# Kernel tuning notes

Hardware: AMD Instinct MI355X
Metric: run time of the kernel (lower is better)

Reference implementation:

```python
import jax, jax.numpy as jnp
import numpy as np

K_BASE = 8
K_MAX = 20
NUM_GROUPS = 16  # min(32, 64 // 4)
EPS = 1e-5


def _knn_idx_adaptive(x, mask, k_base=K_BASE, k_max=K_MAX):
    # x: [B, N, D] float, mask: [B, N] bool. Returns idx: [B, N, k_max] int32.
    B, N, D = x.shape
    x2 = jnp.sum(x * x, axis=-1, keepdims=True)              # [B, N, 1]
    dist2 = x2 + x2.transpose(0, 2, 1) - 2.0 * jnp.einsum('bnd,bmd->bnm', x, x)
    dist2 = jnp.clip(dist2, 0.0)
    valid = mask[:, :, None] & mask[:, None, :]
    eye = jnp.eye(N, dtype=bool)[None]
    dist2 = jnp.where(valid & ~eye, dist2, jnp.inf)
    counts = mask.sum(axis=1)                                 # [B]
    k_per = jnp.clip(jnp.sqrt(counts.astype(jnp.float32) / 50.0) * k_base,
                     k_base, k_max).astype(jnp.int32)         # truncation == torch .long()
    k_global = jnp.minimum(k_max, jnp.maximum(1, counts.min() - 1))
    _, idx = jax.lax.top_k(-dist2, k_max)                     # [B, N, k_max]
    first_valid = jnp.argmax(mask, axis=1)                    # [B]
    cols = jnp.arange(k_max)[None, None, :]
    k_eff = jnp.minimum(k_per, k_global)[:, None, None]
    # cols < k_eff: true top-k neighbors; [k_eff, k_global): repeat first valid; >= k_global: pad 0
    idx = jnp.where(cols < k_eff, idx,
                    jnp.where(cols < k_global, first_valid[:, None, None], 0))
    return idx


def _group_norm(h, gamma, beta, num_groups=NUM_GROUPS, eps=EPS):
    # h: [..., C]
    shp = h.shape
    C = shp[-1]
    hg = h.reshape(shp[:-1] + (num_groups, C // num_groups))
    mu = hg.mean(axis=-1, keepdims=True)
    var = hg.var(axis=-1, keepdims=True)
    hg = (hg - mu) * jax.lax.rsqrt(var + eps)
    return hg.reshape(shp) * gamma + beta


def setup_inputs() -> dict:
    key = jax.random.key(0)
    kx, kl, k1, k2 = jax.random.split(key, 4)
    B, N, D, C = 16, 1024, 64, 64
    x = jax.random.normal(kx, (B, N, D), dtype=jnp.float32)
    lengths = jax.random.randint(kl, (B,), 256, N + 1)
    mask = jnp.arange(N)[None, :] < lengths[:, None]          # [B, N] bool
    W1 = jax.random.normal(k1, (2 * D, C), dtype=jnp.float32) / np.sqrt(2 * D)
    b1 = jnp.zeros((C,), dtype=jnp.float32)
    gamma = jnp.ones((C,), dtype=jnp.float32)
    beta = jnp.zeros((C,), dtype=jnp.float32)
    W2 = jax.random.normal(k2, (C, C), dtype=jnp.float32) / np.sqrt(C)
    b2 = jnp.zeros((C,), dtype=jnp.float32)
    return {"x": x, "mask": mask, "W1": W1, "b1": b1,
            "gamma": gamma, "beta": beta, "W2": W2, "b2": b2}


def reference(x, mask, W1, b1, gamma, beta, W2, b2):
    B, N, D = x.shape
    idx = _knn_idx_adaptive(x, mask)                          # [B, N, k]
    k = idx.shape[-1]
    x_nb = jnp.take_along_axis(x[:, :, None, :].repeat(1, axis=2),
                               idx[..., None], axis=1) if False else \
        x[jnp.arange(B)[:, None, None], idx]                  # [B, N, k, D]
    x_i = jnp.broadcast_to(x[:, :, None, :], (B, N, k, D))
    edge = jnp.concatenate([x_i, x_nb - x_i], axis=-1)        # [B, N, k, 2D]
    h = jax.nn.relu(_group_norm(edge @ W1 + b1, gamma, beta)) # [B, N, k, C]
    h = h @ W2 + b2
    out = h.max(axis=2)                                       # [B, N, C]
    return out * mask[..., None].astype(out.dtype)
```

## Files before the change

kernel.cpp:

```cpp
#include <hip/hip_runtime.h>
#include <stdint.h>

#define BB 16
#define NN 1024
#define DD 64
#define CC 64
#define KMAX 20
#define ROWS 8

typedef unsigned long long u64;
typedef float f32x2 __attribute__((ext_vector_type(2)));
typedef float f32x4v __attribute__((ext_vector_type(4)));
typedef short bf16x8 __attribute__((ext_vector_type(8)));

__device__ inline u64 umin64(u64 a, u64 b) { return a < b ? a : b; }

__device__ inline u64 bitonic_sort64(u64 v, int lane) {
#pragma unroll
    for (int k = 2; k <= 64; k <<= 1) {
#pragma unroll
        for (int j = k >> 1; j > 0; j >>= 1) {
            u64 o = __shfl_xor(v, j);
            bool keepmin = (((lane & j) == 0) == ((lane & k) == 0));
            bool take = ((o < v) == keepmin);
            v = take ? o : v;
        }
    }
    return v;
}

__device__ inline unsigned f2bf(float f) {
    unsigned u = __float_as_uint(f);
    return (u + 0x7FFFu + ((u >> 16) & 1u)) >> 16;
}

__device__ inline bf16x8 pack8(const float4 a, const float4 b) {
    union { unsigned u[4]; bf16x8 v; } r;
    r.u[0] = f2bf(a.x) | (f2bf(a.y) << 16);
    r.u[1] = f2bf(a.z) | (f2bf(a.w) << 16);
    r.u[2] = f2bf(b.x) | (f2bf(b.y) << 16);
    r.u[3] = f2bf(b.z) | (f2bf(b.w) << 16);
    return r.v;
}

__device__ inline void gn4(float4& h, const float4 g, const float4 be) {
    float mu = (h.x + h.y + h.z + h.w) * 0.25f;
    float dx = h.x - mu, dy = h.y - mu, dz = h.z - mu, dw = h.w - mu;
    float var = (dx * dx + dy * dy + dz * dz + dw * dw) * 0.25f;
    float rs = __builtin_amdgcn_rsqf(var + 1e-5f);
    h.x = fmaxf(fmaf(dx * rs, g.x, be.x), 0.f);
    h.y = fmaxf(fmaf(dy * rs, g.y, be.y), 0.f);
    h.z = fmaxf(fmaf(dz * rs, g.z, be.z), 0.f);
    h.w = fmaxf(fmaf(dw * rs, g.w, be.w), 0.f);
}

__global__ void k1_feats(const float* __restrict__ x, const float* __restrict__ W1,
                         const float* __restrict__ b1, float* __restrict__ base,
                         float* __restrict__ fb, float* __restrict__ x2,
                         float* __restrict__ xT, const void* __restrict__ maskp,
                         int* __restrict__ counts, int* __restrict__ keff) {
    __shared__ float sXT[DD][4];
    __shared__ int scnt[BB];
    int w = threadIdx.x >> 6, lane = threadIdx.x & 63;
    int p = blockIdx.x * 4 + w;
    const float* xp = x + (size_t)p * DD;
    float xv = xp[lane];
    float sq = xv * xv;
    for (int off = 32; off; off >>= 1) sq += __shfl_xor(sq, off);
    if (lane == 0) x2[p] = sq;
    sXT[lane][w] = xv;
    float4 xr4[16];
#pragma unroll
    for (int t4 = 0; t4 < 16; ++t4) xr4[t4] = ((const float4*)xp)[t4];
    f32x2 acc2 = {0.f, 0.f};
#pragma unroll
    for (int d = 0; d < DD; ++d) {
        float xd = ((const float*)xr4)[d];
        f32x2 wv = {W1[d * CC + lane], W1[(DD + d) * CC + lane]};
        f32x2 xd2 = {xd, xd};
        acc2 = __builtin_elementwise_fma(xd2, wv, acc2);
    }
    base[(size_t)p * CC + lane] = acc2.x - acc2.y + b1[lane];
    fb[(size_t)p * CC + lane] = acc2.y;
    __syncthreads();
    int t = threadIdx.x;
    int d = t >> 2, po = t & 3;
    int p0 = blockIdx.x * 4;
    int b = p0 >> 10, nb = p0 & 1023;
    xT[(((size_t)(b << 6) + d) << 10) + nb + po] = sXT[d][po];

    if (blockIdx.x == 0) {
        const unsigned char* mb = (const unsigned char*)maskp;
        const int* mi = (const int*)maskp;
        bool bytelayout = (mb[1] != 0);
        for (int bq = 0; bq < 4; ++bq) {
            int bb = w * 4 + bq;
            int s = 0;
            for (int i = 0; i < 16; ++i) {
                int nn2 = lane + (i << 6);
                int v = bytelayout ? (mb[bb * NN + nn2] ? 1 : 0)
                                   : (mi[bb * NN + nn2] ? 1 : 0);
                s += v;
            }
            for (int off = 32; off; off >>= 1) s += __shfl_xor(s, off);
            if (lane == 0) scnt[bb] = s;
        }
        __syncthreads();
        if (t < BB) {
            int minc = scnt[0];
            for (int q = 1; q < BB; ++q) minc = min(minc, scnt[q]);
            int kglob = min(KMAX, max(1, minc - 1));
            float c = (float)scnt[t];
            float v = sqrtf(c / 50.0f) * 8.0f;
            v = fminf(fmaxf(v, 8.0f), 20.0f);
            int kper = (int)v;
            counts[t] = scnt[t];
            keff[t] = min(kper, kglob);
        }
    }
}

#define CE(a, b)                                                      \
    {                                                                 \
        bool sw_ = pk[b] < pk[a];                                     \
        u64 ta_ = pk[a];                                              \
        pk[a] = sw_ ? pk[b] : pk[a];                                  \
        pk[b] = sw_ ? ta_ : pk[b];                                    \
    }

#define ROWFMA(r, rv, cv)                                                        \
    {                                                                            \
        axy[r] = __builtin_elementwise_fma((f32x2){rv, rv}, (f32x2){cv.x, cv.y}, \
                                           axy[r]);                              \
        azw[r] = __builtin_elementwise_fma((f32x2){rv, rv}, (f32x2){cv.z, cv.w}, \
                                           azw[r]);                              \
    }

__global__ __launch_bounds__(256) void k2_knn(const float* __restrict__ x,
                                              const float* __restrict__ xT,
                                              const float* __restrict__ x2,
                                              const int* __restrict__ counts,
                                              const int* __restrict__ keff,
                                              int* __restrict__ idx) {
    __shared__ float sD[ROWS][NN];
    __shared__ float sX2[NN];
    __shared__ u64 sSv[4][64];
    int b = blockIdx.x >> 7;
    int n0 = (blockIdx.x & 127) * ROWS;
    int cnt = counts[b];
    if (n0 >= cnt) return;
    int kef = keff[b];
    int w = threadIdx.x >> 6, lane = threadIdx.x & 63;
    int t = threadIdx.x;
    *(float4*)&sX2[t << 2] = *(const float4*)(x2 + (b << 10) + (t << 2));
    __syncthreads();

    if ((w << 8) < cnt) {
        f32x2 axy[ROWS], azw[ROWS];
#pragma unroll
        for (int r = 0; r < ROWS; ++r) { axy[r] = (f32x2){0.f, 0.f}; azw[r] = (f32x2){0.f, 0.f}; }
        const float* xTb = xT + ((size_t)b << 16);
        const float* xrow0 = x + ((size_t)(b << 10) + n0) * DD;
        int c0 = (w << 8) + (lane << 2);
        for (int d0 = 0; d0 < DD; d0 += 4) {
            float4 cv0 = *(const float4*)(xTb + ((size_t)(d0 + 0) << 10) + c0);
            float4 cv1 = *(const float4*)(xTb + ((size_t)(d0 + 1) << 10) + c0);
            float4 cv2 = *(const float4*)(xTb + ((size_t)(d0 + 2) << 10) + c0);
            float4 cv3 = *(const float4*)(xTb + ((size_t)(d0 + 3) << 10) + c0);
#pragma unroll
            for (int r = 0; r < ROWS; ++r) {
                float4 rv = *(const float4*)(xrow0 + r * DD + d0);
                ROWFMA(r, rv.x, cv0)
                ROWFMA(r, rv.y, cv1)
                ROWFMA(r, rv.z, cv2)
                ROWFMA(r, rv.w, cv3)
            }
        }
#pragma unroll
        for (int r = 0; r < ROWS; ++r)
            *(float4*)&sD[r][c0] = make_float4(axy[r].x, axy[r].y, azw[r].x, azw[r].y);
    }
    __syncthreads();

    for (int rr = 0; rr < 2; ++rr) {
        int r = w + rr * 4;
        int n = n0 + r;
        if (n >= cnt) continue;
        float x2n = sX2[n];
        u64 pk[16];
#pragma unroll
        for (int tt = 0; tt < 16; ++tt) {
            int c = (tt << 6) + lane;
            float dot = sD[r][c];
            float dd = fmaxf((x2n + sX2[c]) - 2.0f * dot, 0.0f);
            pk[tt] = (c < cnt && c != n)
                ? (((u64)__float_as_uint(dd) << 32) | (unsigned)c)
                : ~0ULL;
        }
        u64 h01 = umin64(pk[0], pk[1]),   h23 = umin64(pk[2], pk[3]);
        u64 h45 = umin64(pk[4], pk[5]),   h67 = umin64(pk[6], pk[7]);
        u64 h89 = umin64(pk[8], pk[9]),   hab = umin64(pk[10], pk[11]);
        u64 hcd = umin64(pk[12], pk[13]), hef = umin64(pk[14], pk[15]);
        u64 h = umin64(umin64(umin64(h01, h23), umin64(h45, h67)),
                       umin64(umin64(h89, hab), umin64(hcd, hef)));
        u64 hs = bitonic_sort64(h, lane);
        u64 t0 = __shfl(hs, kef - 1);
        int cle = 0;
#pragma unroll
        for (int i = 0; i < 16; ++i) cle += (pk[i] <= t0) ? 1 : 0;
        int incl = cle;
#pragma unroll
        for (int off = 1; off < 64; off <<= 1) {
            int o = __shfl_up(incl, off);
            incl += (lane >= off) ? o : 0;
        }
        int S = __shfl(incl, 63);
        size_t prow = (size_t)(b << 10) + n;
        if (S <= 64) {
            int pos = incl - cle;
#pragma unroll
            for (int i = 0; i < 16; ++i) {
                if (pk[i] <= t0) { sSv[w][pos] = pk[i]; ++pos; }
            }
            u64 sv = (lane < S) ? sSv[w][lane] : ~0ULL;
            sv = bitonic_sort64(sv, lane);
            if (lane < KMAX)
                idx[prow * KMAX + lane] = (lane < kef) ? (int)(unsigned)(sv & 0xffffffffu) : 0;
        } else {
            CE(0,1) CE(2,3) CE(4,5) CE(6,7) CE(8,9) CE(10,11) CE(12,13) CE(14,15)
            CE(0,2) CE(1,3) CE(4,6) CE(5,7) CE(8,10) CE(9,11) CE(12,14) CE(13,15)
            CE(1,2) CE(5,6) CE(9,10) CE(13,14)
            CE(0,4) CE(1,5) CE(2,6) CE(3,7) CE(8,12) CE(9,13) CE(10,14) CE(11,15)
            CE(2,4) CE(3,5) CE(10,12) CE(11,13)
            CE(1,2) CE(3,4) CE(5,6) CE(9,10) CE(11,12) CE(13,14)
            CE(0,8) CE(1,9) CE(2,10) CE(3,11) CE(4,12) CE(5,13) CE(6,14) CE(7,15)
            CE(4,8) CE(5,9) CE(6,10) CE(7,11)
            CE(2,4) CE(3,5) CE(6,8) CE(7,9) CE(10,12) CE(11,13)
            CE(1,2) CE(3,4) CE(5,6) CE(7,8) CE(9,10) CE(11,12) CE(13,14)
            u64 myhead = pk[0];
            int my_m = 0;
            for (int j = 0; j < kef; ++j) {
                u64 g = myhead;
                for (int off = 32; off; off >>= 1) {
                    u64 o = __shfl_xor(g, off);
                    g = (o < g) ? o : g;
                }
                my_m = (j == lane) ? (int)(unsigned)(g & 0xffffffffu) : my_m;
                bool win = (myhead == g);
#pragma unroll
                for (int tt = 0; tt < 15; ++tt) pk[tt] = win ? pk[tt + 1] : pk[tt];
                pk[15] = win ? ~0ULL : pk[15];
                myhead = pk[0];
            }
            if (lane < KMAX)
                idx[prow * KMAX + lane] = (lane < kef) ? my_m : 0;
        }
    }
}

__global__ __launch_bounds__(256, 2) void k3_mlp(const float* __restrict__ base,
                                                 const float* __restrict__ fb,
                                                 const int* __restrict__ idx,
                                                 const int* __restrict__ counts,
                                                 const float* __restrict__ gamma,
                                                 const float* __restrict__ beta,
                                                 const float* __restrict__ W2,
                                                 const float* __restrict__ b2,
                                                 float* __restrict__ out) {
    __shared__ float sC[4][64][20];
    int w = threadIdx.x >> 6, lane = threadIdx.x & 63;
    int lg = lane >> 4, lr = lane & 15;
    int p0 = blockIdx.x * 16;
    int b = p0 >> 10;
    int n0b = p0 & 1023;
    int cnt = counts[b];
    int pt = p0 + lr;
    bool aval = (n0b + lr) < cnt;

    bf16x8 Bf[4][2];
#pragma unroll
    for (int nt = 0; nt < 4; ++nt)
#pragma unroll
        for (int kt = 0; kt < 2; ++kt) {
            float4 lo, hi;
            const float* wp = W2 + (size_t)(kt * 32 + lg * 8) * CC + nt * 16 + lr;
            lo.x = wp[0 * CC]; lo.y = wp[1 * CC]; lo.z = wp[2 * CC]; lo.w = wp[3 * CC];
            hi.x = wp[4 * CC]; hi.y = wp[5 * CC]; hi.z = wp[6 * CC]; hi.w = wp[7 * CC];
            Bf[nt][kt] = pack8(lo, hi);
        }

    const float* bp = base + (size_t)pt * CC + lg * 8;
    float4 baA0 = *(const float4*)(bp);
    float4 baA1 = *(const float4*)(bp + 4);
    float4 baB0 = *(const float4*)(bp + 32);
    float4 baB1 = *(const float4*)(bp + 36);
    const float* gp = gamma + lg * 8;
    float4 gA0 = *(const float4*)(gp),      gA1 = *(const float4*)(gp + 4);
    float4 gB0 = *(const float4*)(gp + 32), gB1 = *(const float4*)(gp + 36);
    const float* bep = beta + lg * 8;
    float4 eA0 = *(const float4*)(bep),      eA1 = *(const float4*)(bep + 4);
    float4 eB0 = *(const float4*)(bep + 32), eB1 = *(const float4*)(bep + 36);

    const float* fbb = fb + ((size_t)(b << 10)) * CC;
    const int* idxp = idx + (size_t)pt * KMAX;

    f32x4v cmax[4];
#pragma unroll
    for (int nt = 0; nt < 4; ++nt) cmax[nt] = (f32x4v){-1e30f, -1e30f, -1e30f, -1e30f};

#pragma unroll
    for (int jj = 0; jj < 5; ++jj) {
        int j = w * 5 + jj;
        int m = aval ? idxp[j] : 0;
        const float* fr = fbb + (size_t)m * CC + lg * 8;
        float4 hA0 = *(const float4*)(fr);
        float4 hA1 = *(const float4*)(fr + 4);
        float4 hB0 = *(const float4*)(fr + 32);
        float4 hB1 = *(const float4*)(fr + 36);
        hA0.x += baA0.x; hA0.y += baA0.y; hA0.z += baA0.z; hA0.w += baA0.w;
        hA1.x += baA1.x; hA1.y += baA1.y; hA1.z += baA1.z; hA1.w += baA1.w;
        hB0.x += baB0.x; hB0.y += baB0.y; hB0.z += baB0.z; hB0.w += baB0.w;
        hB1.x += baB1.x; hB1.y += baB1.y; hB1.z += baB1.z; hB1.w += baB1.w;
        gn4(hA0, gA0, eA0);
        gn4(hA1, gA1, eA1);
        gn4(hB0, gB0, eB0);
        gn4(hB1, gB1, eB1);
        bf16x8 A0 = pack8(hA0, hA1);
        bf16x8 A1 = pack8(hB0, hB1);
#pragma unroll
        for (int nt = 0; nt < 4; ++nt) {
            f32x4v c = {0.f, 0.f, 0.f, 0.f};
            c = __builtin_amdgcn_mfma_f32_16x16x32_bf16(A0, Bf[nt][0], c, 0, 0, 0);
            c = __builtin_amdgcn_mfma_f32_16x16x32_bf16(A1, Bf[nt][1], c, 0, 0, 0);
            cmax[nt].x = fmaxf(cmax[nt].x, c.x);
            cmax[nt].y = fmaxf(cmax[nt].y, c.y);
            cmax[nt].z = fmaxf(cmax[nt].z, c.z);
            cmax[nt].w = fmaxf(cmax[nt].w, c.w);
        }
    }
#pragma unroll
    for (int nt = 0; nt < 4; ++nt)
        *(float4*)&sC[w][lane][nt * 4] = (float4){cmax[nt].x, cmax[nt].y, cmax[nt].z, cmax[nt].w};
    __syncthreads();
    float b2c = b2[lane];
#pragma unroll
    for (int q = 0; q < 4; ++q) {
        int R = w * 4 + q;
        int src = ((R >> 2) << 4) + lr;
        int reg = (lg << 2) + (R & 3);
        float v = fmaxf(fmaxf(sC[0][src][reg], sC[1][src][reg]),
                        fmaxf(sC[2][src][reg], sC[3][src][reg]));
        bool valid = (n0b + R) < cnt;
        out[(size_t)(p0 + R) * CC + lane] = valid ? (v + b2c) : 0.f;
    }
}

extern "C" void kernel_launch(void* const* d_in, const int* in_sizes, int n_in,
                              void* d_out, int out_size, void* d_ws, size_t ws_size,
                              hipStream_t stream) {
    const float* x     = (const float*)d_in[0];
    const void*  maskp = d_in[1];
    const float* W1    = (const float*)d_in[2];
    const float* b1    = (const float*)d_in[3];
    const float* gamma = (const float*)d_in[4];
    const float* beta  = (const float*)d_in[5];
    const float* W2    = (const float*)d_in[6];
    const float* b2    = (const float*)d_in[7];
    float* out = (float*)d_out;

    int* d_counts = (int*)d_ws;
    int* d_keff   = d_counts + 16;
    float* d_x2   = (float*)(d_counts + 32);
    float* d_base = d_x2 + BB * NN;
    float* d_fb   = d_base + (size_t)BB * NN * CC;
    int* d_idx    = (int*)(d_fb + (size_t)BB * NN * CC);
    float* d_xT   = (float*)d_out;

    hipLaunchKernelGGL(k1_feats, dim3(BB * NN / 4), dim3(256), 0, stream,
                       x, W1, b1, d_base, d_fb, d_x2, d_xT, maskp, d_counts, d_keff);
    hipLaunchKernelGGL(k2_knn, dim3(BB * (NN / ROWS)), dim3(256), 0, stream,
                       x, d_xT, d_x2, d_counts, d_keff, d_idx);
    hipLaunchKernelGGL(k3_mlp, dim3(BB * NN / 16), dim3(256), 0, stream,
                       d_base, d_fb, d_idx, d_counts, gamma, beta, W2, b2, out);
}
```

Before: 100.4 us.

## Reuse W1 in registers across points and replace bitonic sort with radix select

```diff
diff --git a/kernel.cpp b/kernel.cpp
--- a/kernel.cpp
+++ b/kernel.cpp
@@ -7,6 +7,7 @@
 #define CC 64
 #define KMAX 20
 #define ROWS 8
+#define PW 8
 
 typedef unsigned long long u64;
 typedef float f32x2 __attribute__((ext_vector_type(2)));
@@ -54,40 +55,59 @@
     h.w = fmaxf(fmaf(dw * rs, g.w, be.w), 0.f);
 }
 
-__global__ void k1_feats(const float* __restrict__ x, const float* __restrict__ W1,
-                         const float* __restrict__ b1, float* __restrict__ base,
-                         float* __restrict__ fb, float* __restrict__ x2,
-                         float* __restrict__ xT, const void* __restrict__ maskp,
-                         int* __restrict__ counts, int* __restrict__ keff) {
-    __shared__ float sXT[DD][4];
+__global__ __launch_bounds__(256) void k1_feats(const float* __restrict__ x,
+                                                const float* __restrict__ W1,
+                                                const float* __restrict__ b1,
+                                                float* __restrict__ base,
+                                                float* __restrict__ fb,
+                                                float* __restrict__ x2,
+                                                float* __restrict__ xT,
+                                                const void* __restrict__ maskp,
+                                                int* __restrict__ counts,
+                                                int* __restrict__ keff) {
+    __shared__ float sXT[32][65];
     __shared__ int scnt[BB];
     int w = threadIdx.x >> 6, lane = threadIdx.x & 63;
-    int p = blockIdx.x * 4 + w;
-    const float* xp = x + (size_t)p * DD;
-    float xv = xp[lane];
-    float sq = xv * xv;
-    for (int off = 32; off; off >>= 1) sq += __shfl_xor(sq, off);
-    if (lane == 0) x2[p] = sq;
-    sXT[lane][w] = xv;
-    float4 xr4[16];
-#pragma unroll
-    for (int t4 = 0; t4 < 16; ++t4) xr4[t4] = ((const float4*)xp)[t4];
-    f32x2 acc2 = {0.f, 0.f};
+    int p0 = blockIdx.x * 32;
+    int pw0 = p0 + w * PW;
+
+    float w1a[DD], w1b[DD];
 #pragma unroll
     for (int d = 0; d < DD; ++d) {
-        float xd = ((const float*)xr4)[d];
-        f32x2 wv = {W1[d * CC + lane], W1[(DD + d) * CC + lane]};
-        f32x2 xd2 = {xd, xd};
-        acc2 = __builtin_elementwise_fma(xd2, wv, acc2);
-    }
-    base[(size_t)p * CC + lane] = acc2.x - acc2.y + b1[lane];
-    fb[(size_t)p * CC + lane] = acc2.y;
+        w1a[d] = W1[d * CC + lane];
+        w1b[d] = W1[(DD + d) * CC + lane];
+    }
+    float b1c = b1[lane];
+
+#pragma unroll
+    for (int q = 0; q < PW; ++q) {
+        int p_s = __builtin_amdgcn_readfirstlane(pw0 + q);
+        const float* xp = x + (size_t)p_s * DD;
+        float xv = xp[lane];
+        float sq = xv * xv;
+        for (int off = 32; off; off >>= 1) sq += __shfl_xor(sq, off);
+        if (lane == 0) x2[p_s] = sq;
+        sXT[w * PW + q][lane] = xv;
+        f32x2 acc2 = {0.f, 0.f};
+#pragma unroll
+        for (int d = 0; d < DD; ++d) {
+            float xd = xp[d];
+            acc2 = __builtin_elementwise_fma((f32x2){xd, xd},
+                                             (f32x2){w1a[d], w1b[d]}, acc2);
+        }
+        base[(size_t)p_s * CC + lane] = acc2.x - acc2.y + b1c;
+        fb[(size_t)p_s * CC + lane] = acc2.y;
+    }
     __syncthreads();
-    int t = threadIdx.x;
-    int d = t >> 2, po = t & 3;
-    int p0 = blockIdx.x * 4;
-    int b = p0 >> 10, nb = p0 & 1023;
-    xT[(((size_t)(b << 6) + d) << 10) + nb + po] = sXT[d][po];
+    {
+        int b = p0 >> 10, nb = p0 & 1023;
+#pragma unroll
+        for (int i = 0; i < 8; ++i) {
+            int d = i * 8 + (threadIdx.x >> 5);
+            int pt = threadIdx.x & 31;
+            xT[(((size_t)(b << 6) + d) << 10) + nb + pt] = sXT[pt][d];
+        }
+    }
 
     if (blockIdx.x == 0) {
         const unsigned char* mb = (const unsigned char*)maskp;
@@ -106,9 +126,10 @@
             if (lane == 0) scnt[bb] = s;
         }
         __syncthreads();
+        int t = threadIdx.x;
         if (t < BB) {
             int minc = scnt[0];
-            for (int q = 1; q < BB; ++q) minc = min(minc, scnt[q]);
+            for (int qq = 1; qq < BB; ++qq) minc = min(minc, scnt[qq]);
             int kglob = min(KMAX, max(1, minc - 1));
             float c = (float)scnt[t];
             float v = sqrtf(c / 50.0f) * 8.0f;
@@ -203,8 +224,19 @@
         u64 hcd = umin64(pk[12], pk[13]), hef = umin64(pk[14], pk[15]);
         u64 h = umin64(umin64(umin64(h01, h23), umin64(h45, h67)),
                        umin64(umin64(h89, hab), umin64(hcd, hef)));
-        u64 hs = bitonic_sort64(h, lane);
-        u64 t0 = __shfl(hs, kef - 1);
+        unsigned h32 = (unsigned)(h >> 32);
+        unsigned prefix = 0u;
+        int rank = kef;
+#pragma unroll
+        for (int bbit = 31; bbit >= 0; --bbit) {
+            unsigned bitm = 1u << bbit;
+            bool cand0 = ((((u64)(h32 ^ prefix)) >> (bbit + 1)) == 0) &&
+                         ((h32 & bitm) == 0);
+            u64 m0 = __ballot(cand0);
+            int c0 = __popcll(m0);
+            if (rank > c0) { rank -= c0; prefix |= bitm; }
+        }
+        u64 t0 = (((u64)prefix) << 32) | 0xFFFFFFFFULL;
         int cle = 0;
 #pragma unroll
         for (int i = 0; i < 16; ++i) cle += (pk[i] <= t0) ? 1 : 0;
@@ -376,7 +408,7 @@
     int* d_idx    = (int*)(d_fb + (size_t)BB * NN * CC);
     float* d_xT   = (float*)d_out;
 
-    hipLaunchKernelGGL(k1_feats, dim3(BB * NN / 4), dim3(256), 0, stream,
+    hipLaunchKernelGGL(k1_feats, dim3(BB * NN / 32), dim3(256), 0, stream,
                        x, W1, b1, d_base, d_fb, d_x2, d_xT, maskp, d_counts, d_keff);
     hipLaunchKernelGGL(k2_knn, dim3(BB * (NN / ROWS)), dim3(256), 0, stream,
                        x, d_xT, d_x2, d_counts, d_keff, d_idx);
```

Result: faster. 96.30 us (-4.1%).
